# Performance work log

Hardware: AMD Instinct MI355X
Metric: run time of the kernel (lower is better)

The kernel has to match this reference:

```python
import jax, jax.numpy as jnp
import numpy as np

K = 3
STRIDE = 1
PAD = 1


def _conv2d(x, w, b):
    y = jax.lax.conv_general_dilated(
        x, w, window_strides=(STRIDE, STRIDE),
        padding=[(PAD, PAD), (PAD, PAD)],
        dimension_numbers=("NCHW", "OIHW", "NCHW"))
    return y + b[None, :, None, None]


def _bilinear_sample(xb, py, px):
    # xb: [C, H, W]; py, px: [K2, Ho, Wo] float sample coords
    C, H, W = xb.shape
    y0 = jnp.floor(py)
    x0 = jnp.floor(px)
    ay = py - y0  # frac weights
    ax = px - x0
    out = jnp.zeros((C,) + py.shape, dtype=xb.dtype)
    corners = [
        (y0, x0, (1.0 - ay) * (1.0 - ax)),
        (y0, x0 + 1.0, (1.0 - ay) * ax),
        (y0 + 1.0, x0, ay * (1.0 - ax)),
        (y0 + 1.0, x0 + 1.0, ay * ax),
    ]
    for yc, xc, wgt in corners:
        valid = (yc >= 0) & (yc < H) & (xc >= 0) & (xc < W)
        yi = jnp.clip(yc, 0, H - 1).astype(jnp.int32)
        xi = jnp.clip(xc, 0, W - 1).astype(jnp.int32)
        g = xb[:, yi, xi]  # [C, K2, Ho, Wo]
        out = out + g * (wgt * valid.astype(xb.dtype))[None]
    return out


def _deform_forward(x, weight, bias, p_weight, p_bias):
    B, Cin, H, W = x.shape
    Cout = weight.shape[0]
    K2 = K * K
    # offset / mask prediction conv
    pout = _conv2d(x, p_weight, p_bias)  # [B, 3*K2, Ho, Wo]
    o1, o2, m = jnp.split(pout, 3, axis=1)
    offset = jnp.concatenate([o1, o2], axis=1)  # [B, 2*K2, Ho, Wo]
    mask = jax.nn.sigmoid(m)  # [B, K2, Ho, Wo]
    Ho, Wo = mask.shape[2], mask.shape[3]
    # torchvision layout: channel 2k = dy_k, 2k+1 = dx_k
    off = offset.reshape(B, K2, 2, Ho, Wo)
    dy, dx = off[:, :, 0], off[:, :, 1]  # [B, K2, Ho, Wo]
    ki = (jnp.arange(K2) // K).astype(x.dtype)  # kernel row
    kj = (jnp.arange(K2) % K).astype(x.dtype)   # kernel col
    base_y = jnp.arange(Ho, dtype=x.dtype) * STRIDE - PAD  # [Ho]
    base_x = jnp.arange(Wo, dtype=x.dtype) * STRIDE - PAD  # [Wo]
    py = base_y[None, None, :, None] + ki[None, :, None, None] + dy
    px = base_x[None, None, None, :] + kj[None, :, None, None] + dx
    sampled = jax.vmap(_bilinear_sample)(x, py, px)  # [B, Cin, K2, Ho, Wo]
    sampled = sampled * mask[:, None]
    w = weight.reshape(Cout, Cin, K2)
    out = jnp.einsum('bckhw,ock->bohw', sampled, w) + bias[None, :, None, None]
    return out


def setup_inputs() -> dict:
    key = jax.random.key(0)
    k1, k2, k3 = jax.random.split(key, 3)
    B, Cin, Cout, H, W = 4, 256, 256, 64, 64
    x = jax.random.normal(k1, (B, Cin, H, W), dtype=jnp.float32)
    fan_in = Cin * K * K
    weight = jax.random.normal(k2, (Cout, Cin, K, K), dtype=jnp.float32) / np.sqrt(fan_in)
    bias = jnp.zeros((Cout,), dtype=jnp.float32)
    # small random offset/mask predictor (zero-init in the original; randomized
    # here so the deformable sampling path is exercised)
    p_weight = jax.random.normal(k3, (3 * K * K, Cin, K, K), dtype=jnp.float32) * 0.02
    p_bias = jnp.zeros((3 * K * K,), dtype=jnp.float32)
    return {"x": x, "weight": weight, "bias": bias, "p_weight": p_weight, "p_bias": p_bias}


def reference(x, weight, bias, p_weight, p_bias):
    return _deform_forward(x, weight, bias, p_weight, p_bias)
```

## Files before the change

kernel.cpp:

```cpp
#include <hip/hip_runtime.h>
#include <stdint.h>


#define CIN 256
#define COUT 256
#define HWS 4096
#define MTOT 16384
#define KTOT 2304
#define SPLITK 8

typedef __attribute__((ext_vector_type(8))) short bf16x8;
typedef __attribute__((ext_vector_type(4))) float f32x4;

__device__ __forceinline__ unsigned short f2bf(float f) {
  unsigned int u = __float_as_uint(f);
  unsigned int r = (u + 0x7fffu + ((u >> 16) & 1u)) >> 16;
  return (unsigned short)r;
}
__device__ __forceinline__ float bf2f(unsigned short u) {
  return __uint_as_float(((unsigned int)u) << 16);
}
__device__ __forceinline__ float bflo(unsigned int u) { return __uint_as_float(u << 16); }
__device__ __forceinline__ float bfhi(unsigned int u) { return __uint_as_float(u & 0xffff0000u); }

__device__ __forceinline__ void gload_lds16(const void* g, void* l) {
  __builtin_amdgcn_global_load_lds((const __attribute__((address_space(1))) void*)g,
                                   (__attribute__((address_space(3))) void*)l, 16, 0, 0);
}

__global__ __launch_bounds__(256) void prep_and_transpose(const float* __restrict__ x,
                                                          const float* __restrict__ w,
                                                          const float* __restrict__ pw,
                                                          unsigned short* __restrict__ xt,
                                                          unsigned short* __restrict__ WB,
                                                          unsigned short* __restrict__ PWs,
                                                          unsigned short* __restrict__ zerop) {
  __shared__ float tile[32][33];
  int bid = blockIdx.x;
  if (bid < 4096) {
    int b = bid >> 10;
    int rest = bid & 1023;
    int hw0 = (rest & 127) * 32;
    int c0 = ((rest >> 7) & 7) * 32;
    int tx = threadIdx.x & 31, ty = threadIdx.x >> 5;
    for (int i = ty; i < 32; i += 8)
      tile[i][tx] = x[(size_t)(b * CIN + c0 + i) * HWS + hw0 + tx];
    __syncthreads();
    for (int r = ty; r < 32; r += 8)
      xt[(size_t)(b * HWS + hw0 + r) * CIN + c0 + tx] = f2bf(tile[tx][r]);
  } else {
    int idx = (bid - 4096) * 256 + threadIdx.x;
    if (idx < 512)
      *(uint4*)(zerop + idx * 8) = make_uint4(0, 0, 0, 0);
    if (idx < KTOT * COUT) {
      int f = idx;
      int e = f & 7;
      int row = (f >> 3) & 15;
      int quad = (f >> 7) & 3;
      int j = (f >> 9) & 15;
      int t = f >> 13;
      int kk = t * 32 + quad * 8 + e;
      int o = j * 16 + row;
      int k = kk >> 8, c = kk & 255;
      WB[f] = f2bf(w[o * KTOT + c * 9 + k]);
    } else {
      int f2 = idx - KTOT * COUT;
      int t_ = f2 & 7;
      int rest = f2 >> 3;
      int j = rest & 31;
      int kk = (rest >> 5) * 8 + t_;
      int k = kk >> 8, c = kk & 255;
      float v = (j < 27) ? pw[j * KTOT + c * 9 + k] : 0.0f;
      PWs[f2] = f2bf(v);
    }
  }
}

__global__ __launch_bounds__(256) void offset_conv_sk(const unsigned short* __restrict__ xt,
                                                      const unsigned short* __restrict__ PWs,
                                                      const unsigned short* __restrict__ zerop,
                                                      float* __restrict__ Pbuf) {
  __shared__ unsigned short Al[64 * 32];
  __shared__ unsigned short Bl[1024];
  int tid = threadIdx.x;
  int lane = tid & 63, wv = tid >> 6;
  int mt = (blockIdx.x & 7) * 32 + (blockIdx.x >> 3);
  int m0 = mt * 64;
  int s = blockIdx.y;
  int b = m0 >> 12;
  int hw0 = m0 & 4095;
  f32x4 acc[2] = {};

  for (int tt = 0; tt < 72 / SPLITK; ++tt) {
    int t = s * (72 / SPLITK) + tt;
    int k = t >> 3, c0 = (t & 7) * 32;
    int dyk = k / 3 - 1;
    int dxk = k % 3 - 1;
    __syncthreads();
    if (tid < 128)
      gload_lds16(PWs + (size_t)t * 1024 + tid * 8, &Bl[tid * 8]);
    {
      int r = tid >> 2;
      int hw = hw0 + r;
      int h = hw >> 6, wwp = hw & 63;
      int y = h + dyk, xx = wwp + dxk;
      bool valid = ((unsigned)y < 64u) && ((unsigned)xx < 64u);
      const unsigned short* src = valid
          ? xt + ((size_t)((b << 12) + (y << 6) + xx) << 8) + c0 + (tid & 3) * 8
          : zerop;
      gload_lds16(src, &Al[tid * 8]);
    }
    __syncthreads();
    int row = lane & 15, quad = lane >> 4;
    bf16x8 af = *(const bf16x8*)&Al[(wv * 16 + row) * 32 + quad * 8];
    for (int j = 0; j < 2; ++j) {
      bf16x8 bfr = *(const bf16x8*)&Bl[(quad * 32 + j * 16 + row) * 8];
      acc[j] = __builtin_amdgcn_mfma_f32_16x16x32_bf16(af, bfr, acc[j], 0, 0, 0);
    }
  }

  int row = lane & 15, quad = lane >> 4;
  for (int j = 0; j < 2; ++j) {
    int n = j * 16 + row;
    for (int r_ = 0; r_ < 4; ++r_) {
      int m = m0 + wv * 16 + quad * 4 + r_;
      Pbuf[((size_t)s * MTOT + m) * 32 + n] = acc[j][r_];
    }
  }
}

__global__ __launch_bounds__(256) void index_prep(const float* __restrict__ Pbuf,
                                                  const float* __restrict__ p_bias,
                                                  int4* __restrict__ DIW) {
  int gid = blockIdx.x * 256 + threadIdx.x;
  int m = gid / 9;
  int k = gid - m * 9;

  float dy = p_bias[2 * k];
  float dx = p_bias[2 * k + 1];
  float mv = p_bias[18 + k];
#pragma unroll
  for (int s = 0; s < SPLITK; ++s) {
    const float* p = Pbuf + ((size_t)s * MTOT + m) * 32;
    dy += p[2 * k];
    dx += p[2 * k + 1];
    mv += p[18 + k];
  }
  float mk = 1.0f / (1.0f + __expf(-mv));

  int hw = m & 4095, h = hw >> 6, ww = hw & 63;
  float py = (float)(h - 1 + k / 3) + dy;
  float px = (float)(ww - 1 + k % 3) + dx;
  float y0f = floorf(py), x0f = floorf(px);
  float ay = py - y0f, ax = px - x0f;
  int y0 = (int)y0f, x0 = (int)x0f;

  float w00 = (1.f - ay) * (1.f - ax) * mk;
  float w01 = (1.f - ay) * ax * mk;
  float w10 = ay * (1.f - ax) * mk;
  float w11 = ay * ax * mk;

  float vy0 = ((unsigned)y0 < 64u) ? 1.f : 0.f;
  float vy1 = ((unsigned)(y0 + 1) < 64u) ? 1.f : 0.f;
  float vx0 = ((unsigned)x0 < 64u) ? 1.f : 0.f;
  float vx1 = ((unsigned)(x0 + 1) < 64u) ? 1.f : 0.f;
  w00 *= vy0 * vx0; w01 *= vy0 * vx1; w10 *= vy1 * vx0; w11 *= vy1 * vx1;

  int yc0 = min(max(y0, 0), 63), yc1 = min(max(y0 + 1, 0), 63);
  int xc0 = min(max(x0, 0), 63), xc1 = min(max(x0 + 1, 0), 63);

  DIW[(size_t)gid * 2] = make_int4((yc0 * 64 + xc0) * 256, (yc0 * 64 + xc1) * 256,
                                   (yc1 * 64 + xc0) * 256, (yc1 * 64 + xc1) * 256);
  float4 w4 = make_float4(w00, w01, w10, w11);
  ((float4*)DIW)[(size_t)gid * 2 + 1] = w4;
}

__device__ __forceinline__ void bilin4p(const uint2 c00, const uint2 c01,
                                        const uint2 c10, const uint2 c11,
                                        const float4 w4, unsigned short* dst) {
  float v0 = w4.x * bflo(c00.x) + w4.y * bflo(c01.x) + w4.z * bflo(c10.x) + w4.w * bflo(c11.x);
  float v1 = w4.x * bfhi(c00.x) + w4.y * bfhi(c01.x) + w4.z * bfhi(c10.x) + w4.w * bfhi(c11.x);
  float v2 = w4.x * bflo(c00.y) + w4.y * bflo(c01.y) + w4.z * bflo(c10.y) + w4.w * bflo(c11.y);
  float v3 = w4.x * bfhi(c00.y) + w4.y * bfhi(c01.y) + w4.z * bfhi(c10.y) + w4.w * bfhi(c11.y);
  ushort4 o;
  o.x = f2bf(v0); o.y = f2bf(v1); o.z = f2bf(v2); o.w = f2bf(v3);
  *(ushort4*)dst = o;
}

#define MFMA8(A0, A1, A2_, A3, B0, B1)                                                   \
  acc[0][0] = __builtin_amdgcn_mfma_f32_16x16x32_bf16(A0, B0, acc[0][0], 0, 0, 0);       \
  acc[0][1] = __builtin_amdgcn_mfma_f32_16x16x32_bf16(A0, B1, acc[0][1], 0, 0, 0);       \
  acc[1][0] = __builtin_amdgcn_mfma_f32_16x16x32_bf16(A1, B0, acc[1][0], 0, 0, 0);       \
  acc[1][1] = __builtin_amdgcn_mfma_f32_16x16x32_bf16(A1, B1, acc[1][1], 0, 0, 0);       \
  acc[2][0] = __builtin_amdgcn_mfma_f32_16x16x32_bf16(A2_, B0, acc[2][0], 0, 0, 0);      \
  acc[2][1] = __builtin_amdgcn_mfma_f32_16x16x32_bf16(A2_, B1, acc[2][1], 0, 0, 0);      \
  acc[3][0] = __builtin_amdgcn_mfma_f32_16x16x32_bf16(A3, B0, acc[3][0], 0, 0, 0);       \
  acc[3][1] = __builtin_amdgcn_mfma_f32_16x16x32_bf16(A3, B1, acc[3][1], 0, 0, 0);

#define FITER(T, PAR, BC0, BC1, BN0, BN1)                                                \
  {                                                                                      \
    if ((T) <= 69) {                                                                     \
      if ((((T) + 2) & 7) == 0) dI4 = Tbl[r][((T) + 2) >> 3][0];                         \
      int cq = (((T) + 2) & 7) * 32 + qo;                                                \
      g00 = *(const uint2*)(xtb + dI4.x + cq);                                           \
      g01 = *(const uint2*)(xtb + dI4.y + cq);                                           \
      g10 = *(const uint2*)(xtb + dI4.z + cq);                                           \
      g11 = *(const uint2*)(xtb + dI4.w + cq);                                           \
    }                                                                                    \
    if ((T) <= 70) {                                                                     \
      const unsigned short* bt_ = bpb + (size_t)((T) + 1) * 8192;                        \
      BN0 = *(const bf16x8*)(bt_);                                                       \
      BN1 = *(const bf16x8*)(bt_ + 512);                                                 \
    }                                                                                    \
    afr0 = *(const bf16x8*)&As[PAR][row][quad * 8];                                      \
    afr1 = *(const bf16x8*)&As[PAR][16 + row][quad * 8];                                 \
    afr2 = *(const bf16x8*)&As[PAR][32 + row][quad * 8];                                 \
    afr3 = *(const bf16x8*)&As[PAR][48 + row][quad * 8];                                 \
    if ((T) <= 70) {                                                                     \
      if ((((T) + 1) & 7) == 0) dW4 = *(float4*)&Tbl[r][((T) + 1) >> 3][1];              \
      bilin4p(gp0, gp1, gp2, gp3, dW4, &As[PAR ^ 1][r][qo]);                             \
    }                                                                                    \
    MFMA8(afr0, afr1, afr2, afr3, BC0, BC1)                                              \
    __syncthreads();                                                                     \
  }

__global__ __launch_bounds__(512, 2) void fused_gemm(const unsigned short* __restrict__ xt,
                                                     const int4* __restrict__ DIW,
                                                     const unsigned short* __restrict__ WB,
                                                     const float* __restrict__ bias,
                                                     float* __restrict__ out) {
  __shared__ unsigned short As[2][64][40];
  __shared__ int4 Tbl[64][9][2];

  int tid = threadIdx.x;
  int lane = tid & 63, wv = tid >> 6;
  int mt = (blockIdx.x & 7) * 32 + (blockIdx.x >> 3);
  int mb = mt * 64;
  int b = mb >> 12;
  int hw0 = mb & 4095;
  const unsigned short* xtb = xt + ((size_t)b << 20);

  {
    const int4* src = DIW + (size_t)mb * 18;
    int4* dst = (int4*)Tbl;
    for (int i = tid; i < 1152; i += 512)
      gload_lds16(src + i, dst + i);
  }
  __syncthreads();

  int r = tid >> 3;
  int qo = (tid & 7) * 4;

  int4 dI4 = Tbl[r][0][0];
  float4 dW4 = *(float4*)&Tbl[r][0][1];

  int row = lane & 15, quad = lane >> 4;
  const unsigned short* bpb = WB + (size_t)(wv * 2) * 512 + quad * 128 + row * 8;

  f32x4 acc[4][2] = {};
  uint2 g00, g01, g10, g11;
  uint2 gp0, gp1, gp2, gp3;
  bf16x8 bA0, bA1, bB0, bB1;
  bf16x8 afr0, afr1, afr2, afr3;

  {
    g00 = *(const uint2*)(xtb + dI4.x + qo);
    g01 = *(const uint2*)(xtb + dI4.y + qo);
    g10 = *(const uint2*)(xtb + dI4.z + qo);
    g11 = *(const uint2*)(xtb + dI4.w + qo);
    bA0 = *(const bf16x8*)(bpb);
    bA1 = *(const bf16x8*)(bpb + 512);
    bilin4p(g00, g01, g10, g11, dW4, &As[0][r][qo]);
    g00 = *(const uint2*)(xtb + dI4.x + 32 + qo);
    g01 = *(const uint2*)(xtb + dI4.y + 32 + qo);
    g10 = *(const uint2*)(xtb + dI4.z + 32 + qo);
    g11 = *(const uint2*)(xtb + dI4.w + 32 + qo);
  }
  __syncthreads();

#pragma unroll 1
  for (int t = 0; t < 72; t += 2) {
    gp0 = g00; gp1 = g01; gp2 = g10; gp3 = g11;
    FITER(t, 0, bA0, bA1, bB0, bB1)
    gp0 = g00; gp1 = g01; gp2 = g10; gp3 = g11;
    FITER(t + 1, 1, bB0, bB1, bA0, bA1)
  }

#pragma unroll
  for (int j = 0; j < 2; ++j) {
    int o = wv * 32 + j * 16 + row;
    float bo = bias[o];
#pragma unroll
    for (int i = 0; i < 4; ++i) {
      int hw = hw0 + i * 16 + quad * 4;
      float4 v;
      v.x = acc[i][j][0] + bo;
      v.y = acc[i][j][1] + bo;
      v.z = acc[i][j][2] + bo;
      v.w = acc[i][j][3] + bo;
      *(float4*)(out + (((size_t)(b * COUT + o)) << 12) + hw) = v;
    }
  }
}

extern "C" void kernel_launch(void* const* d_in, const int* in_sizes, int n_in,
                              void* d_out, int out_size, void* d_ws, size_t ws_size,
                              hipStream_t stream) {
  const float* x        = (const float*)d_in[0];
  const float* weight   = (const float*)d_in[1];
  const float* bias     = (const float*)d_in[2];
  const float* p_weight = (const float*)d_in[3];
  const float* p_bias   = (const float*)d_in[4];
  float* out = (float*)d_out;
  char* ws = (char*)d_ws;

  const size_t OFF_XT   = 0;
  const size_t OFF_WB   = OFF_XT + 8388608;
  const size_t OFF_PW   = OFF_WB + 1179648;
  const size_t OFF_P    = OFF_PW + 147456;
  const size_t OFF_ZP   = OFF_P + 16777216;
  const size_t OFF_DIW  = OFF_ZP + 8192;

  unsigned short* xt    = (unsigned short*)(ws + OFF_XT);
  unsigned short* WB    = (unsigned short*)(ws + OFF_WB);
  unsigned short* PWs   = (unsigned short*)(ws + OFF_PW);
  float* Pbuf           = (float*)(ws + OFF_P);
  unsigned short* zerop = (unsigned short*)(ws + OFF_ZP);
  int4* DIW             = (int4*)(ws + OFF_DIW);

  prep_and_transpose<<<4096 + 2592, 256, 0, stream>>>(x, weight, p_weight, xt, WB, PWs, zerop);
  offset_conv_sk<<<dim3(MTOT / 64, SPLITK), 256, 0, stream>>>(xt, PWs, zerop, Pbuf);
  index_prep<<<576, 256, 0, stream>>>(Pbuf, p_bias, DIW);
  fused_gemm<<<256, 512, 0, stream>>>(xt, DIW, WB, bias, out);
}
```

Baseline: 150.6 us.

## Use inline-asm global loads with explicit vmcnt waits in fused GEMM pipeline

Replaces compiler-generated global loads in the main loop with inline asm loads into ping-pong register sets, and uses explicit s_waitcnt vmcnt counters so each stage waits only for the loads it needs while newer prefetches stay in flight. The loop is restructured to remove per-iteration conditionals by peeling the last two iterations. The barrier is replaced with an lgkmcnt wait plus s_barrier, which no longer drains outstanding vector memory loads. Hand-counted vmcnt values are fragile: any extra global load the compiler schedules in between would make them wrong.

```diff
diff --git a/kernel.cpp b/kernel.cpp
--- a/kernel.cpp
+++ b/kernel.cpp
@@ -27,6 +27,16 @@
   __builtin_amdgcn_global_load_lds((const __attribute__((address_space(1))) void*)g,
                                    (__attribute__((address_space(3))) void*)l, 16, 0, 0);
 }
+
+#define GLOAD8(D, P)  asm volatile("global_load_dwordx2 %0, %1, off" : "=v"(D) : "v"(P))
+#define GLOAD16(D, P) asm volatile("global_load_dwordx4 %0, %1, off" : "=v"(D) : "v"(P))
+#define WAITVM(N)                                            \
+  {                                                          \
+    asm volatile("s_waitcnt vmcnt(" #N ")" ::: "memory");    \
+    __builtin_amdgcn_sched_barrier(0);                       \
+  }
+#define BARRIER_LGKM                                                  \
+  { asm volatile("s_waitcnt lgkmcnt(0)\n\ts_barrier" ::: "memory"); }
 
 __global__ __launch_bounds__(256) void prep_and_transpose(const float* __restrict__ x,
                                                           const float* __restrict__ w,
@@ -197,31 +207,27 @@
   acc[3][0] = __builtin_amdgcn_mfma_f32_16x16x32_bf16(A3, B0, acc[3][0], 0, 0, 0);       \
   acc[3][1] = __builtin_amdgcn_mfma_f32_16x16x32_bf16(A3, B1, acc[3][1], 0, 0, 0);
 
-#define FITER(T, PAR, BC0, BC1, BN0, BN1)                                                \
+#define FITER_S(T, PAR, GI0, GI1, GI2, GI3, GC0, GC1, GC2, GC3, BC0, BC1, BN0, BN1)      \
   {                                                                                      \
-    if ((T) <= 69) {                                                                     \
-      if ((((T) + 2) & 7) == 0) dI4 = Tbl[r][((T) + 2) >> 3][0];                         \
-      int cq = (((T) + 2) & 7) * 32 + qo;                                                \
-      g00 = *(const uint2*)(xtb + dI4.x + cq);                                           \
-      g01 = *(const uint2*)(xtb + dI4.y + cq);                                           \
-      g10 = *(const uint2*)(xtb + dI4.z + cq);                                           \
-      g11 = *(const uint2*)(xtb + dI4.w + cq);                                           \
-    }                                                                                    \
-    if ((T) <= 70) {                                                                     \
-      const unsigned short* bt_ = bpb + (size_t)((T) + 1) * 8192;                        \
-      BN0 = *(const bf16x8*)(bt_);                                                       \
-      BN1 = *(const bf16x8*)(bt_ + 512);                                                 \
-    }                                                                                    \
+    if ((((T) + 2) & 7) == 0) dI4 = Tbl[r][((T) + 2) >> 3][0];                           \
+    int cq = (((T) + 2) & 7) * 32 + qo;                                                  \
+    GLOAD8(GI0, xtb + dI4.x + cq);                                                       \
+    GLOAD8(GI1, xtb + dI4.y + cq);                                                       \
+    GLOAD8(GI2, xtb + dI4.z + cq);                                                       \
+    GLOAD8(GI3, xtb + dI4.w + cq);                                                       \
+    const unsigned short* bt_ = bpb + (size_t)((T) + 1) * 8192;                          \
+    GLOAD16(BN0, bt_);                                                                   \
+    GLOAD16(BN1, bt_ + 512);                                                             \
     afr0 = *(const bf16x8*)&As[PAR][row][quad * 8];                                      \
     afr1 = *(const bf16x8*)&As[PAR][16 + row][quad * 8];                                 \
     afr2 = *(const bf16x8*)&As[PAR][32 + row][quad * 8];                                 \
     afr3 = *(const bf16x8*)&As[PAR][48 + row][quad * 8];                                 \
-    if ((T) <= 70) {                                                                     \
-      if ((((T) + 1) & 7) == 0) dW4 = *(float4*)&Tbl[r][((T) + 1) >> 3][1];              \
-      bilin4p(gp0, gp1, gp2, gp3, dW4, &As[PAR ^ 1][r][qo]);                             \
-    }                                                                                    \
+    if ((((T) + 1) & 7) == 0) dW4 = *(float4*)&Tbl[r][((T) + 1) >> 3][1];                \
+    WAITVM(8)                                                                            \
+    bilin4p(GC0, GC1, GC2, GC3, dW4, &As[PAR ^ 1][r][qo]);                               \
+    WAITVM(6)                                                                            \
     MFMA8(afr0, afr1, afr2, afr3, BC0, BC1)                                              \
-    __syncthreads();                                                                     \
+    BARRIER_LGKM                                                                         \
   }
 
 __global__ __launch_bounds__(512, 2) void fused_gemm(const unsigned short* __restrict__ xt,
@@ -258,32 +264,53 @@
   const unsigned short* bpb = WB + (size_t)(wv * 2) * 512 + quad * 128 + row * 8;
 
   f32x4 acc[4][2] = {};
-  uint2 g00, g01, g10, g11;
-  uint2 gp0, gp1, gp2, gp3;
+  uint2 gA0, gA1, gA2, gA3;
+  uint2 gB0, gB1, gB2, gB3;
   bf16x8 bA0, bA1, bB0, bB1;
   bf16x8 afr0, afr1, afr2, afr3;
 
   {
-    g00 = *(const uint2*)(xtb + dI4.x + qo);
-    g01 = *(const uint2*)(xtb + dI4.y + qo);
-    g10 = *(const uint2*)(xtb + dI4.z + qo);
-    g11 = *(const uint2*)(xtb + dI4.w + qo);
-    bA0 = *(const bf16x8*)(bpb);
-    bA1 = *(const bf16x8*)(bpb + 512);
-    bilin4p(g00, g01, g10, g11, dW4, &As[0][r][qo]);
-    g00 = *(const uint2*)(xtb + dI4.x + 32 + qo);
-    g01 = *(const uint2*)(xtb + dI4.y + 32 + qo);
-    g10 = *(const uint2*)(xtb + dI4.z + 32 + qo);
-    g11 = *(const uint2*)(xtb + dI4.w + 32 + qo);
-  }
-  __syncthreads();
+    uint2 p00 = *(const uint2*)(xtb + dI4.x + qo);
+    uint2 p01 = *(const uint2*)(xtb + dI4.y + qo);
+    uint2 p10 = *(const uint2*)(xtb + dI4.z + qo);
+    uint2 p11 = *(const uint2*)(xtb + dI4.w + qo);
+    bilin4p(p00, p01, p10, p11, dW4, &As[0][r][qo]);
+    GLOAD8(gB0, xtb + dI4.x + 32 + qo);
+    GLOAD8(gB1, xtb + dI4.y + 32 + qo);
+    GLOAD8(gB2, xtb + dI4.z + 32 + qo);
+    GLOAD8(gB3, xtb + dI4.w + 32 + qo);
+    GLOAD16(bA0, bpb);
+    GLOAD16(bA1, bpb + 512);
+  }
+  BARRIER_LGKM
 
 #pragma unroll 1
-  for (int t = 0; t < 72; t += 2) {
-    gp0 = g00; gp1 = g01; gp2 = g10; gp3 = g11;
-    FITER(t, 0, bA0, bA1, bB0, bB1)
-    gp0 = g00; gp1 = g01; gp2 = g10; gp3 = g11;
-    FITER(t + 1, 1, bB0, bB1, bA0, bA1)
+  for (int t = 0; t < 70; t += 2) {
+    FITER_S(t,     0, gA0, gA1, gA2, gA3, gB0, gB1, gB2, gB3, bA0, bA1, bB0, bB1)
+    FITER_S(t + 1, 1, gB0, gB1, gB2, gB3, gA0, gA1, gA2, gA3, bB0, bB1, bA0, bA1)
+  }
+
+  {
+    const unsigned short* bt_ = bpb + (size_t)71 * 8192;
+    GLOAD16(bB0, bt_);
+    GLOAD16(bB1, bt_ + 512);
+    afr0 = *(const bf16x8*)&As[0][row][quad * 8];
+    afr1 = *(const bf16x8*)&As[0][16 + row][quad * 8];
+    afr2 = *(const bf16x8*)&As[0][32 + row][quad * 8];
+    afr3 = *(const bf16x8*)&As[0][48 + row][quad * 8];
+    WAITVM(4)
+    bilin4p(gB0, gB1, gB2, gB3, dW4, &As[1][r][qo]);
+    WAITVM(2)
+    MFMA8(afr0, afr1, afr2, afr3, bA0, bA1)
+    BARRIER_LGKM
+  }
+  {
+    afr0 = *(const bf16x8*)&As[1][row][quad * 8];
+    afr1 = *(const bf16x8*)&As[1][16 + row][quad * 8];
+    afr2 = *(const bf16x8*)&As[1][32 + row][quad * 8];
+    afr3 = *(const bf16x8*)&As[1][48 + row][quad * 8];
+    WAITVM(0)
+    MFMA8(afr0, afr1, afr2, afr3, bB0, bB1)
   }
 
 #pragma unroll
```

Result: faster. 133.7 us (-11.2%).

## Build A fragments in registers and give each wave all output channels

Applied to the files above, without the earlier changes.

The fused GEMM no longer stages bilinearly sampled A tiles in shared memory. Each lane now gathers 8 channels with uint4 loads and forms its MFMA A fragment directly in registers, which removes the LDS round trip and the per-iteration __syncthreads. Each wave now owns 16 rows and all 256 output channels (16 accumulators), and the block shrinks to 256 threads with launch bounds (256,1). The cost is 32 B-fragment registers per lane for double buffering, much higher register pressure, lower occupancy, and every wave loading the full weight slice per k-step.

```diff
diff --git a/kernel.cpp b/kernel.cpp
--- a/kernel.cpp
+++ b/kernel.cpp
@@ -175,61 +175,84 @@
   ((float4*)DIW)[(size_t)gid * 2 + 1] = w4;
 }
 
-__device__ __forceinline__ void bilin4p(const uint2 c00, const uint2 c01,
-                                        const uint2 c10, const uint2 c11,
-                                        const float4 w4, unsigned short* dst) {
-  float v0 = w4.x * bflo(c00.x) + w4.y * bflo(c01.x) + w4.z * bflo(c10.x) + w4.w * bflo(c11.x);
-  float v1 = w4.x * bfhi(c00.x) + w4.y * bfhi(c01.x) + w4.z * bfhi(c10.x) + w4.w * bfhi(c11.x);
-  float v2 = w4.x * bflo(c00.y) + w4.y * bflo(c01.y) + w4.z * bflo(c10.y) + w4.w * bflo(c11.y);
-  float v3 = w4.x * bfhi(c00.y) + w4.y * bfhi(c01.y) + w4.z * bfhi(c10.y) + w4.w * bfhi(c11.y);
-  ushort4 o;
-  o.x = f2bf(v0); o.y = f2bf(v1); o.z = f2bf(v2); o.w = f2bf(v3);
-  *(ushort4*)dst = o;
-}
-
-#define MFMA8(A0, A1, A2_, A3, B0, B1)                                                   \
-  acc[0][0] = __builtin_amdgcn_mfma_f32_16x16x32_bf16(A0, B0, acc[0][0], 0, 0, 0);       \
-  acc[0][1] = __builtin_amdgcn_mfma_f32_16x16x32_bf16(A0, B1, acc[0][1], 0, 0, 0);       \
-  acc[1][0] = __builtin_amdgcn_mfma_f32_16x16x32_bf16(A1, B0, acc[1][0], 0, 0, 0);       \
-  acc[1][1] = __builtin_amdgcn_mfma_f32_16x16x32_bf16(A1, B1, acc[1][1], 0, 0, 0);       \
-  acc[2][0] = __builtin_amdgcn_mfma_f32_16x16x32_bf16(A2_, B0, acc[2][0], 0, 0, 0);      \
-  acc[2][1] = __builtin_amdgcn_mfma_f32_16x16x32_bf16(A2_, B1, acc[2][1], 0, 0, 0);      \
-  acc[3][0] = __builtin_amdgcn_mfma_f32_16x16x32_bf16(A3, B0, acc[3][0], 0, 0, 0);       \
-  acc[3][1] = __builtin_amdgcn_mfma_f32_16x16x32_bf16(A3, B1, acc[3][1], 0, 0, 0);
-
-#define FITER(T, PAR, BC0, BC1, BN0, BN1)                                                \
-  {                                                                                      \
-    if ((T) <= 69) {                                                                     \
-      if ((((T) + 2) & 7) == 0) dI4 = Tbl[r][((T) + 2) >> 3][0];                         \
-      int cq = (((T) + 2) & 7) * 32 + qo;                                                \
-      g00 = *(const uint2*)(xtb + dI4.x + cq);                                           \
-      g01 = *(const uint2*)(xtb + dI4.y + cq);                                           \
-      g10 = *(const uint2*)(xtb + dI4.z + cq);                                           \
-      g11 = *(const uint2*)(xtb + dI4.w + cq);                                           \
-    }                                                                                    \
-    if ((T) <= 70) {                                                                     \
-      const unsigned short* bt_ = bpb + (size_t)((T) + 1) * 8192;                        \
-      BN0 = *(const bf16x8*)(bt_);                                                       \
-      BN1 = *(const bf16x8*)(bt_ + 512);                                                 \
-    }                                                                                    \
-    afr0 = *(const bf16x8*)&As[PAR][row][quad * 8];                                      \
-    afr1 = *(const bf16x8*)&As[PAR][16 + row][quad * 8];                                 \
-    afr2 = *(const bf16x8*)&As[PAR][32 + row][quad * 8];                                 \
-    afr3 = *(const bf16x8*)&As[PAR][48 + row][quad * 8];                                 \
-    if ((T) <= 70) {                                                                     \
-      if ((((T) + 1) & 7) == 0) dW4 = *(float4*)&Tbl[r][((T) + 1) >> 3][1];              \
-      bilin4p(gp0, gp1, gp2, gp3, dW4, &As[PAR ^ 1][r][qo]);                             \
-    }                                                                                    \
-    MFMA8(afr0, afr1, afr2, afr3, BC0, BC1)                                              \
-    __syncthreads();                                                                     \
-  }
-
-__global__ __launch_bounds__(512, 2) void fused_gemm(const unsigned short* __restrict__ xt,
+__device__ __forceinline__ bf16x8 bilin8r(const uint4 c00, const uint4 c01,
+                                          const uint4 c10, const uint4 c11,
+                                          const float4 w4) {
+  uint4 o;
+  float v0, v1;
+  v0 = w4.x * bflo(c00.x) + w4.y * bflo(c01.x) + w4.z * bflo(c10.x) + w4.w * bflo(c11.x);
+  v1 = w4.x * bfhi(c00.x) + w4.y * bfhi(c01.x) + w4.z * bfhi(c10.x) + w4.w * bfhi(c11.x);
+  o.x = (unsigned)f2bf(v0) | ((unsigned)f2bf(v1) << 16);
+  v0 = w4.x * bflo(c00.y) + w4.y * bflo(c01.y) + w4.z * bflo(c10.y) + w4.w * bflo(c11.y);
+  v1 = w4.x * bfhi(c00.y) + w4.y * bfhi(c01.y) + w4.z * bfhi(c10.y) + w4.w * bfhi(c11.y);
+  o.y = (unsigned)f2bf(v0) | ((unsigned)f2bf(v1) << 16);
+  v0 = w4.x * bflo(c00.z) + w4.y * bflo(c01.z) + w4.z * bflo(c10.z) + w4.w * bflo(c11.z);
+  v1 = w4.x * bfhi(c00.z) + w4.y * bfhi(c01.z) + w4.z * bfhi(c10.z) + w4.w * bfhi(c11.z);
+  o.z = (unsigned)f2bf(v0) | ((unsigned)f2bf(v1) << 16);
+  v0 = w4.x * bflo(c00.w) + w4.y * bflo(c01.w) + w4.z * bflo(c10.w) + w4.w * bflo(c11.w);
+  v1 = w4.x * bfhi(c00.w) + w4.y * bfhi(c01.w) + w4.z * bfhi(c10.w) + w4.w * bfhi(c11.w);
+  o.w = (unsigned)f2bf(v0) | ((unsigned)f2bf(v1) << 16);
+  return *(bf16x8*)&o;
+}
+
+#define MFMA16J(AC, BC)                                                                   \
+  acc[0]  = __builtin_amdgcn_mfma_f32_16x16x32_bf16(AC, BC##0,  acc[0],  0, 0, 0);        \
+  acc[1]  = __builtin_amdgcn_mfma_f32_16x16x32_bf16(AC, BC##1,  acc[1],  0, 0, 0);        \
+  acc[2]  = __builtin_amdgcn_mfma_f32_16x16x32_bf16(AC, BC##2,  acc[2],  0, 0, 0);        \
+  acc[3]  = __builtin_amdgcn_mfma_f32_16x16x32_bf16(AC, BC##3,  acc[3],  0, 0, 0);        \
+  acc[4]  = __builtin_amdgcn_mfma_f32_16x16x32_bf16(AC, BC##4,  acc[4],  0, 0, 0);        \
+  acc[5]  = __builtin_amdgcn_mfma_f32_16x16x32_bf16(AC, BC##5,  acc[5],  0, 0, 0);        \
+  acc[6]  = __builtin_amdgcn_mfma_f32_16x16x32_bf16(AC, BC##6,  acc[6],  0, 0, 0);        \
+  acc[7]  = __builtin_amdgcn_mfma_f32_16x16x32_bf16(AC, BC##7,  acc[7],  0, 0, 0);        \
+  acc[8]  = __builtin_amdgcn_mfma_f32_16x16x32_bf16(AC, BC##8,  acc[8],  0, 0, 0);        \
+  acc[9]  = __builtin_amdgcn_mfma_f32_16x16x32_bf16(AC, BC##9,  acc[9],  0, 0, 0);        \
+  acc[10] = __builtin_amdgcn_mfma_f32_16x16x32_bf16(AC, BC##10, acc[10], 0, 0, 0);        \
+  acc[11] = __builtin_amdgcn_mfma_f32_16x16x32_bf16(AC, BC##11, acc[11], 0, 0, 0);        \
+  acc[12] = __builtin_amdgcn_mfma_f32_16x16x32_bf16(AC, BC##12, acc[12], 0, 0, 0);        \
+  acc[13] = __builtin_amdgcn_mfma_f32_16x16x32_bf16(AC, BC##13, acc[13], 0, 0, 0);        \
+  acc[14] = __builtin_amdgcn_mfma_f32_16x16x32_bf16(AC, BC##14, acc[14], 0, 0, 0);        \
+  acc[15] = __builtin_amdgcn_mfma_f32_16x16x32_bf16(AC, BC##15, acc[15], 0, 0, 0);
+
+#define LOADB16(BI, PTR)                                                                  \
+  {                                                                                       \
+    const unsigned short* b_ = (PTR);                                                     \
+    BI##0  = *(const bf16x8*)(b_);                                                        \
+    BI##1  = *(const bf16x8*)(b_ + 512);                                                  \
+    BI##2  = *(const bf16x8*)(b_ + 1024);                                                 \
+    BI##3  = *(const bf16x8*)(b_ + 1536);                                                 \
+    BI##4  = *(const bf16x8*)(b_ + 2048);                                                 \
+    BI##5  = *(const bf16x8*)(b_ + 2560);                                                 \
+    BI##6  = *(const bf16x8*)(b_ + 3072);                                                 \
+    BI##7  = *(const bf16x8*)(b_ + 3584);                                                 \
+    BI##8  = *(const bf16x8*)(b_ + 4096);                                                 \
+    BI##9  = *(const bf16x8*)(b_ + 4608);                                                 \
+    BI##10 = *(const bf16x8*)(b_ + 5120);                                                 \
+    BI##11 = *(const bf16x8*)(b_ + 5632);                                                 \
+    BI##12 = *(const bf16x8*)(b_ + 6144);                                                 \
+    BI##13 = *(const bf16x8*)(b_ + 6656);                                                 \
+    BI##14 = *(const bf16x8*)(b_ + 7168);                                                 \
+    BI##15 = *(const bf16x8*)(b_ + 7680);                                                 \
+  }
+
+#define FITER(T, BC, BI, GC, GI, AC, AN)                                                  \
+  {                                                                                       \
+    LOADB16(BI, btb + (size_t)((T) + 1) * 8192)                                           \
+    if ((((T) + 2) & 7) == 0) dI4 = Tbl[mr][((T) + 2) >> 3][0];                           \
+    int cb = (((T) + 2) & 7) * 32 + kq8;                                                  \
+    GI##0 = *(const uint4*)(xtb + dI4.x + cb);                                            \
+    GI##1 = *(const uint4*)(xtb + dI4.y + cb);                                            \
+    GI##2 = *(const uint4*)(xtb + dI4.z + cb);                                            \
+    GI##3 = *(const uint4*)(xtb + dI4.w + cb);                                            \
+    if ((((T) + 1) & 7) == 0) dW4 = *(float4*)&Tbl[mr][((T) + 1) >> 3][1];                \
+    MFMA16J(AC, BC)                                                                       \
+    AN = bilin8r(GC##0, GC##1, GC##2, GC##3, dW4);                                        \
+  }
+
+__global__ __launch_bounds__(256, 1) void fused_gemm(const unsigned short* __restrict__ xt,
                                                      const int4* __restrict__ DIW,
                                                      const unsigned short* __restrict__ WB,
                                                      const float* __restrict__ bias,
                                                      float* __restrict__ out) {
-  __shared__ unsigned short As[2][64][40];
   __shared__ int4 Tbl[64][9][2];
 
   int tid = threadIdx.x;
@@ -237,69 +260,74 @@
   int mt = (blockIdx.x & 7) * 32 + (blockIdx.x >> 3);
   int mb = mt * 64;
   int b = mb >> 12;
-  int hw0 = mb & 4095;
   const unsigned short* xtb = xt + ((size_t)b << 20);
 
   {
     const int4* src = DIW + (size_t)mb * 18;
     int4* dst = (int4*)Tbl;
-    for (int i = tid; i < 1152; i += 512)
+    for (int i = tid; i < 1152; i += 256)
       gload_lds16(src + i, dst + i);
   }
   __syncthreads();
 
-  int r = tid >> 3;
-  int qo = (tid & 7) * 4;
-
-  int4 dI4 = Tbl[r][0][0];
-  float4 dW4 = *(float4*)&Tbl[r][0][1];
-
-  int row = lane & 15, quad = lane >> 4;
-  const unsigned short* bpb = WB + (size_t)(wv * 2) * 512 + quad * 128 + row * 8;
-
-  f32x4 acc[4][2] = {};
-  uint2 g00, g01, g10, g11;
-  uint2 gp0, gp1, gp2, gp3;
-  bf16x8 bA0, bA1, bB0, bB1;
-  bf16x8 afr0, afr1, afr2, afr3;
+  int row = lane & 15;
+  int kq = lane >> 4;
+  int kq8 = kq * 8;
+  int mr = wv * 16 + row;
+
+  int4 dI4 = Tbl[mr][0][0];
+  float4 dW4 = *(float4*)&Tbl[mr][0][1];
+
+  const unsigned short* btb = WB + kq * 128 + row * 8;
+
+  f32x4 acc[16] = {};
+  bf16x8 bA0, bA1, bA2, bA3, bA4, bA5, bA6, bA7,
+         bA8, bA9, bA10, bA11, bA12, bA13, bA14, bA15;
+  bf16x8 bB0, bB1, bB2, bB3, bB4, bB5, bB6, bB7,
+         bB8, bB9, bB10, bB11, bB12, bB13, bB14, bB15;
+  uint4 gA0, gA1, gA2, gA3, gB0, gB1, gB2, gB3;
+  bf16x8 afA, afB;
 
   {
-    g00 = *(const uint2*)(xtb + dI4.x + qo);
-    g01 = *(const uint2*)(xtb + dI4.y + qo);
-    g10 = *(const uint2*)(xtb + dI4.z + qo);
-    g11 = *(const uint2*)(xtb + dI4.w + qo);
-    bA0 = *(const bf16x8*)(bpb);
-    bA1 = *(const bf16x8*)(bpb + 512);
-    bilin4p(g00, g01, g10, g11, dW4, &As[0][r][qo]);
-    g00 = *(const uint2*)(xtb + dI4.x + 32 + qo);
-    g01 = *(const uint2*)(xtb + dI4.y + 32 + qo);
-    g10 = *(const uint2*)(xtb + dI4.z + 32 + qo);
-    g11 = *(const uint2*)(xtb + dI4.w + 32 + qo);
-  }
-  __syncthreads();
+    uint4 p00 = *(const uint4*)(xtb + dI4.x + kq8);
+    uint4 p01 = *(const uint4*)(xtb + dI4.y + kq8);
+    uint4 p10 = *(const uint4*)(xtb + dI4.z + kq8);
+    uint4 p11 = *(const uint4*)(xtb + dI4.w + kq8);
+    afA = bilin8r(p00, p01, p10, p11, dW4);
+    LOADB16(bA, btb)
+    int cb1 = 32 + kq8;
+    gA0 = *(const uint4*)(xtb + dI4.x + cb1);
+    gA1 = *(const uint4*)(xtb + dI4.y + cb1);
+    gA2 = *(const uint4*)(xtb + dI4.z + cb1);
+    gA3 = *(const uint4*)(xtb + dI4.w + cb1);
+  }
 
 #pragma unroll 1
-  for (int t = 0; t < 72; t += 2) {
-    gp0 = g00; gp1 = g01; gp2 = g10; gp3 = g11;
-    FITER(t, 0, bA0, bA1, bB0, bB1)
-    gp0 = g00; gp1 = g01; gp2 = g10; gp3 = g11;
-    FITER(t + 1, 1, bB0, bB1, bA0, bA1)
-  }
-
+  for (int t = 0; t < 70; t += 2) {
+    FITER(t,     bA, bB, gA, gB, afA, afB)
+    FITER(t + 1, bB, bA, gB, gA, afB, afA)
+  }
+
+  {
+    LOADB16(bB, btb + (size_t)71 * 8192)
+    MFMA16J(afA, bA)
+    afB = bilin8r(gA0, gA1, gA2, gA3, dW4);
+  }
+  {
+    MFMA16J(afB, bB)
+  }
+
+  int hwb = (mb & 4095) + wv * 16 + kq * 4;
 #pragma unroll
-  for (int j = 0; j < 2; ++j) {
-    int o = wv * 32 + j * 16 + row;
+  for (int j = 0; j < 16; ++j) {
+    int o = j * 16 + row;
     float bo = bias[o];
-#pragma unroll
-    for (int i = 0; i < 4; ++i) {
-      int hw = hw0 + i * 16 + quad * 4;
-      float4 v;
-      v.x = acc[i][j][0] + bo;
-      v.y = acc[i][j][1] + bo;
-      v.z = acc[i][j][2] + bo;
-      v.w = acc[i][j][3] + bo;
-      *(float4*)(out + (((size_t)(b * COUT + o)) << 12) + hw) = v;
-    }
+    float4 v;
+    v.x = acc[j][0] + bo;
+    v.y = acc[j][1] + bo;
+    v.z = acc[j][2] + bo;
+    v.w = acc[j][3] + bo;
+    *(float4*)(out + (((size_t)(b * COUT + o)) << 12) + hwb) = v;
   }
 }
 
@@ -331,5 +359,5 @@
   prep_and_transpose<<<4096 + 2592, 256, 0, stream>>>(x, weight, p_weight, xt, WB, PWs, zerop);
   offset_conv_sk<<<dim3(MTOT / 64, SPLITK), 256, 0, stream>>>(xt, PWs, zerop, Pbuf);
   index_prep<<<576, 256, 0, stream>>>(Pbuf, p_bias, DIW);
-  fused_gemm<<<256, 512, 0, stream>>>(xt, DIW, WB, bias, out);
-}
+  fused_gemm<<<256, 256, 0, stream>>>(xt, DIW, WB, bias, out);
+}
```

After: 163.1 us. +8.3%, slower.
